# Optimization experiments

Hardware: AMD Instinct MI355X
Metric: run time of the kernel (lower is better)

Reference implementation:

```python
import jax, jax.numpy as jnp
import numpy as np

B, N, H = 2, 4096, 1024
HEADS, DHEAD, M = 16, 64, 256
KERNEL_EPS = 1e-3


def setup_inputs() -> dict:
    key = jax.random.key(0)
    ks = jax.random.split(key, 10)
    w = lambda k, shp: jax.random.normal(k, shp, dtype=jnp.float32) * 0.02
    return {
        "hidden_states": jax.random.normal(ks[0], (B, N, H), dtype=jnp.float32),
        "Wq": w(ks[1], (H, H)), "bq": jnp.zeros((H,), jnp.float32),
        "Wk": w(ks[2], (H, H)), "bk": jnp.zeros((H,), jnp.float32),
        "Wv": w(ks[3], (H, H)), "bv": jnp.zeros((H,), jnp.float32),
        "Wo": w(ks[4], (H, H)), "bo": jnp.zeros((H,), jnp.float32),
        "proj": jax.random.normal(ks[5], (M, DHEAD), dtype=jnp.float32),
    }


def _split_heads(x):
    b, n, _ = x.shape
    return x.reshape(b, n, HEADS, DHEAD).transpose(0, 2, 1, 3)  # [b,h,n,d]


def _softmax_kernel(data, proj, is_query):
    # data: [b,h,n,d]; proj: [m,d]
    data_normalizer = DHEAD ** (-0.25)
    data_dash = jnp.einsum('bhnd,md->bhnm', data_normalizer * data, proj)
    diag_data = -0.5 * jnp.sum(data * data, axis=-1, keepdims=True)  # [b,h,n,1]
    if is_query:
        # argmax over a size-1 last dim -> stabilizer == diag_data itself
        stab = diag_data
    else:
        stab = jnp.max(diag_data)
    kernel_out = jnp.exp(diag_data + (data_dash - stab))  # exp kernel: exp(h + x)
    return (M ** (-0.5)) * (kernel_out + KERNEL_EPS)


def _performer_forward(hidden_states, Wq, bq, Wk, bk, Wv, bv, Wo, bo, proj):
    q = _split_heads(jnp.einsum('bni,oi->bno', hidden_states, Wq) + bq)
    k = _split_heads(jnp.einsum('bni,oi->bno', hidden_states, Wk) + bk)
    v = _split_heads(jnp.einsum('bni,oi->bno', hidden_states, Wv) + bv)

    qf = _softmax_kernel(q, proj, is_query=True)   # [b,h,n,m]
    kf = _softmax_kernel(k, proj, is_query=False)  # [b,h,n,m]

    # linear_attention (non-causal FAVOR+)
    k_cumsum = kf.sum(axis=-2)                                   # [b,h,m]
    d_inv = 1.0 / jnp.einsum('bhnm,bhm->bhn', qf, k_cumsum)      # [b,h,n]
    context = jnp.einsum('bhnm,bhne->bhme', kf, v)               # [b,h,m,d]
    out = jnp.einsum('bhme,bhnm,bhn->bhne', context, qf, d_inv)  # [b,h,n,d]

    out = out.transpose(0, 2, 1, 3).reshape(hidden_states.shape[0], -1, H)
    return jnp.einsum('bni,oi->bno', out, Wo) + bo


def reference(hidden_states, Wq, bq, Wk, bk, Wv, bv, Wo, bo, proj):
    return _performer_forward(hidden_states, Wq, bq, Wk, bk, Wv, bv, Wo, bo, proj)
```

## Files before the change

kernel.cpp:

```cpp
#include <hip/hip_runtime.h>
#include <math.h>

#define B_      2
#define N_      4096
#define H_      1024
#define HEADS_  16
#define DH_     64
#define M_      256
#define NSPLIT  8
#define EPAD    80

constexpr float NORMALIZER = 0.35355339059327373f;
constexpr float RATIO      = 0.0625f;
constexpr float KEPS       = 1e-3f;

typedef __bf16 bf16x8 __attribute__((ext_vector_type(8)));
typedef __bf16 bf16x4 __attribute__((ext_vector_type(4)));
typedef float  f32x4  __attribute__((ext_vector_type(4)));

__global__ __launch_bounds__(256) void split_bf16(
    const float* __restrict__ src, __bf16* __restrict__ hi, __bf16* __restrict__ lo)
{
    int i = blockIdx.x * 256 + threadIdx.x;
    float4 v = ((const float4*)src)[i];
    float vv[4] = {v.x, v.y, v.z, v.w};
    bf16x4 h, l;
#pragma unroll
    for (int j = 0; j < 4; ++j) {
        __bf16 hh = (__bf16)vv[j];
        h[j] = hh;
        l[j] = (__bf16)(vv[j] - (float)hh);
    }
    ((bf16x4*)hi)[i] = h;
    ((bf16x4*)lo)[i] = l;
}

__global__ __launch_bounds__(256) void split_w(
    const float* __restrict__ W0, const float* __restrict__ W1,
    const float* __restrict__ W2, const float* __restrict__ W3,
    __bf16* __restrict__ hi, __bf16* __restrict__ lo)
{
    const float* src = W0;
    if (blockIdx.y == 1) src = W1;
    else if (blockIdx.y == 2) src = W2;
    else if (blockIdx.y == 3) src = W3;
    int i = blockIdx.x * 256 + threadIdx.x;
    size_t o = (size_t)blockIdx.y * 262144 + i;
    float4 v = ((const float4*)src)[i];
    float vv[4] = {v.x, v.y, v.z, v.w};
    bf16x4 h, l;
#pragma unroll
    for (int j = 0; j < 4; ++j) {
        __bf16 hh = (__bf16)vv[j];
        h[j] = hh;
        l[j] = (__bf16)(vv[j] - (float)hh);
    }
    ((bf16x4*)hi)[o] = h;
    ((bf16x4*)lo)[o] = l;
}

template<bool BF16OUT>
__global__ __launch_bounds__(512, 4) void gemm_mfma3(
    const __bf16* __restrict__ Ah, const __bf16* __restrict__ Al,
    const __bf16* __restrict__ Bh0, const __bf16* __restrict__ Bl0,
    const __bf16* __restrict__ Bh1, const __bf16* __restrict__ Bl1,
    const __bf16* __restrict__ Bh2, const __bf16* __restrict__ Bl2,
    const float* __restrict__ bi0, const float* __restrict__ bi1, const float* __restrict__ bi2,
    float* __restrict__ C0,
    __bf16* __restrict__ Ch0, __bf16* __restrict__ Cl0,
    __bf16* __restrict__ Ch1, __bf16* __restrict__ Cl1,
    __bf16* __restrict__ Ch2, __bf16* __restrict__ Cl2)
{
    const __bf16* Bh = Bh0; const __bf16* Bl = Bl0; const float* bias = bi0;
    __bf16* Ch = Ch0; __bf16* Cl = Cl0;
    if (blockIdx.z == 1) { Bh = Bh1; Bl = Bl1; bias = bi1; Ch = Ch1; Cl = Cl1; }
    else if (blockIdx.z == 2) { Bh = Bh2; Bl = Bl2; bias = bi2; Ch = Ch2; Cl = Cl2; }

    __shared__ alignas(16) __bf16 lds[2][4][128 * 32];

    const int t    = threadIdx.x;
    const int lane = t & 63;
    const int lm   = lane & 15;
    const int lq   = lane >> 4;
    const int w    = t >> 6;
    const int wm   = (w >> 2) * 64;
    const int wn   = (w & 3) * 32;

    const int wg = blockIdx.x + 8 * blockIdx.y;
    const int sw = (wg & 7) * 64 + (wg >> 3);
    const int n0 = (sw & 7) * 128;
    const int m0 = (sw >> 3) * 128;
    const int K    = 1024;
    const int NK   = 32;

    const int tw = w >> 1;
    const int hw = w & 1;
    const __bf16* mysrc = (tw == 0) ? Ah : (tw == 1) ? Al : (tw == 2) ? Bh : Bl;
    const int     rbase = ((tw < 2) ? m0 : n0) + hw * 64;
    const int rsub   = lane >> 2;
    const int slot   = lane & 3;
    const int schunk = slot ^ ((lane >> 3) & 3);
    const __bf16* gbase = mysrc + (size_t)(rbase + rsub) * K + schunk * 8;

    f32x4 acc[4][2];
#pragma unroll
    for (int i = 0; i < 4; ++i)
#pragma unroll
        for (int j = 0; j < 2; ++j) acc[i][j] = (f32x4){0.f, 0.f, 0.f, 0.f};

    const int swz = (lq ^ ((lm >> 1) & 3)) * 8;

    auto stage = [&](int buf, int k0) {
#pragma unroll
        for (int c = 0; c < 4; ++c) {
            const __bf16* g = gbase + (size_t)c * 16 * K + k0;
            __builtin_amdgcn_global_load_lds(
                (const __attribute__((address_space(1))) void*)g,
                (__attribute__((address_space(3))) void*)&lds[buf][tw][(hw * 64 + c * 16) * 32],
                16, 0, 0);
        }
    };

    auto compute = [&](int p) {
        const __bf16* tAh = lds[p][0];
        const __bf16* tAl = lds[p][1];
        const __bf16* tBh = lds[p][2];
        const __bf16* tBl = lds[p][3];
        bf16x8 bh[2], bl[2];
#pragma unroll
        for (int j = 0; j < 2; ++j) {
            int off = (wn + j * 16 + lm) * 32 + swz;
            bh[j] = *(const bf16x8*)&tBh[off];
            bl[j] = *(const bf16x8*)&tBl[off];
        }
#pragma unroll
        for (int i = 0; i < 4; ++i) {
            int off = (wm + i * 16 + lm) * 32 + swz;
            bf16x8 ah = *(const bf16x8*)&tAh[off];
            bf16x8 al = *(const bf16x8*)&tAl[off];
#pragma unroll
            for (int j = 0; j < 2; ++j) {
                acc[i][j] = __builtin_amdgcn_mfma_f32_16x16x32_bf16(ah, bh[j], acc[i][j], 0, 0, 0);
                acc[i][j] = __builtin_amdgcn_mfma_f32_16x16x32_bf16(al, bh[j], acc[i][j], 0, 0, 0);
                acc[i][j] = __builtin_amdgcn_mfma_f32_16x16x32_bf16(ah, bl[j], acc[i][j], 0, 0, 0);
            }
        }
    };

    stage(0, 0);
    int p = 0;
#pragma unroll 1
    for (int kk = 0; kk < NK - 1; ++kk) {
        stage(p ^ 1, (kk + 1) * 32);
        asm volatile("s_waitcnt vmcnt(4)" ::: "memory");
        asm volatile("s_barrier" ::: "memory");
        compute(p);
        asm volatile("s_barrier" ::: "memory");
        p ^= 1;
    }
    asm volatile("s_waitcnt vmcnt(0)" ::: "memory");
    asm volatile("s_barrier" ::: "memory");
    compute(p);

    float bsr[2];
#pragma unroll
    for (int j = 0; j < 2; ++j) bsr[j] = bias[n0 + wn + j * 16 + lm];
#pragma unroll
    for (int i = 0; i < 4; ++i)
#pragma unroll
        for (int r = 0; r < 4; ++r) {
            int rowm = m0 + wm + i * 16 + lq * 4 + r;
#pragma unroll
            for (int j = 0; j < 2; ++j) {
                int col = n0 + wn + j * 16 + lm;
                float o = acc[i][j][r] + bsr[j];
                if (BF16OUT) {
                    __bf16 hh = (__bf16)o;
                    Ch[(size_t)rowm * 1024 + col] = hh;
                    Cl[(size_t)rowm * 1024 + col] = (__bf16)(o - (float)hh);
                } else {
                    C0[(size_t)rowm * 1024 + col] = o;
                }
            }
        }
}

__global__ __launch_bounds__(256) void diag_kernel(
    const __bf16* __restrict__ Kh, const __bf16* __restrict__ Kl,
    float* __restrict__ diag, float* __restrict__ partials)
{
    int gt = blockIdx.x * 256 + threadIdx.x;
    int r  = gt >> 2;
    int q  = gt & 3;
    const bf16x8* ph = (const bf16x8*)(Kh + (size_t)r * 64 + q * 16);
    const bf16x8* pl = (const bf16x8*)(Kl + (size_t)r * 64 + q * 16);
    float s = 0.f;
#pragma unroll
    for (int i = 0; i < 2; ++i) {
        bf16x8 vh = ph[i], vl = pl[i];
#pragma unroll
        for (int j = 0; j < 8; ++j) {
            float x = (float)vh[j] + (float)vl[j];
            s += x * x;
        }
    }
    s += __shfl_xor(s, 1);
    s += __shfl_xor(s, 2);
    float d = -0.5f * s;
    if (q == 0) {
        int h = r & 15, bn = r >> 4;
        int n = bn & 4095, b = bn >> 12;
        diag[(((size_t)b * 16 + h) << 12) + n] = d;
    }
    __shared__ float red[256];
    red[threadIdx.x] = d;
    __syncthreads();
    for (int s2 = 128; s2 > 0; s2 >>= 1) {
        if (threadIdx.x < s2) red[threadIdx.x] = fmaxf(red[threadIdx.x], red[threadIdx.x + s2]);
        __syncthreads();
    }
    if (threadIdx.x == 0) partials[blockIdx.x] = red[0];
}

__global__ __launch_bounds__(256) void reduce_stab(
    const float* __restrict__ partials, float* __restrict__ stab, int n)
{
    float m = -3.0e38f;
    for (int i = threadIdx.x; i < n; i += 256) m = fmaxf(m, partials[i]);
    __shared__ float red[256];
    red[threadIdx.x] = m;
    __syncthreads();
    for (int s2 = 128; s2 > 0; s2 >>= 1) {
        if (threadIdx.x < s2) red[threadIdx.x] = fmaxf(red[threadIdx.x], red[threadIdx.x + s2]);
        __syncthreads();
    }
    if (threadIdx.x == 0) stab[0] = red[0];
}

__global__ __launch_bounds__(256) void ctx_mfma(
    const __bf16* __restrict__ Kh, const __bf16* __restrict__ Kl,
    const __bf16* __restrict__ Vh, const __bf16* __restrict__ Vl,
    const __bf16* __restrict__ projH, const __bf16* __restrict__ projL,
    const float* __restrict__ diag, const float* __restrict__ stabp,
    float* __restrict__ ctxp)
{
    __shared__ alignas(16) char ldsbuf[59904];
    __shared__ float dg[64];
    __bf16* kfTh = (__bf16*)ldsbuf;
    __bf16* kfTl = kfTh + 9216;
    __bf16* vTh  = kfTl + 9216;
    __bf16* vTl  = vTh + 5760;
    float*  ctxe = (float*)ldsbuf;

    const int t    = threadIdx.x;
    const int lane = t & 63;
    const int w    = t >> 6;
    const int lm   = lane & 15;
    const int lq   = lane >> 4;
    const int bh   = blockIdx.z;
    const int b    = bh >> 4, h = bh & 15;
    const int mh   = blockIdx.y;
    const int slice = blockIdx.x;
    const int mwave = mh * 128 + w * 32;
    const float stab = stabp[0];
    const size_t rowbase = (size_t)b * N_ * H_ + (size_t)h * DH_;
    const float* diag_bh = diag + (size_t)bh * N_;

    for (int idx = t; idx < 16 * 72; idx += 256) {
        int e = 64 + idx / 72, n = idx % 72;
        vTh[e * 72 + n] = (e == 64 && n < 64) ? (__bf16)1.0f : (__bf16)0.0f;
        vTl[e * 72 + n] = (__bf16)0.0f;
    }

    bf16x8 ph[2][2], pl[2][2];
#pragma unroll
    for (int mf = 0; mf < 2; ++mf)
#pragma unroll
        for (int ks = 0; ks < 2; ++ks) {
            size_t pa = (size_t)(mwave + mf * 16 + lm) * 64 + ks * 32 + lq * 8;
            ph[mf][ks] = *(const bf16x8*)(projH + pa);
            pl[mf][ks] = *(const bf16x8*)(projL + pa);
        }

    f32x4 acc[2][5];
#pragma unroll
    for (int mf = 0; mf < 2; ++mf)
#pragma unroll
        for (int ef = 0; ef < 5; ++ef) acc[mf][ef] = (f32x4){0.f, 0.f, 0.f, 0.f};

    const int nl = t >> 2, dc = (t & 3) * 16;
    bf16x8 v0, v1, u0, u1;
    {
        size_t va = rowbase + (size_t)(slice * (N_ / NSPLIT) + nl) * H_ + dc;
        v0 = *(const bf16x8*)(Vh + va);
        v1 = *(const bf16x8*)(Vh + va + 8);
        u0 = *(const bf16x8*)(Vl + va);
        u1 = *(const bf16x8*)(Vl + va + 8);
    }

    for (int tile = 0; tile < 8; ++tile) {
        const int n0 = slice * (N_ / NSPLIT) + tile * 64;
        __syncthreads();

#pragma unroll
        for (int j = 0; j < 8; ++j) {
            vTh[(dc + j) * 72 + nl]     = v0[j];
            vTh[(dc + 8 + j) * 72 + nl] = v1[j];
            vTl[(dc + j) * 72 + nl]     = u0[j];
            vTl[(dc + 8 + j) * 72 + nl] = u1[j];
        }
        if (t < 64) dg[t] = diag_bh[n0 + t] - stab;

        f32x4 dsh[4][2];
#pragma unroll
        for (int nf = 0; nf < 4; ++nf) {
#pragma unroll
            for (int mf = 0; mf < 2; ++mf) dsh[nf][mf] = (f32x4){0.f, 0.f, 0.f, 0.f};
            bf16x8 ah[2], al[2];
#pragma unroll
            for (int ks = 0; ks < 2; ++ks) {
                size_t ka = rowbase + (size_t)(n0 + nf * 16 + lm) * H_ + ks * 32 + lq * 8;
                ah[ks] = *(const bf16x8*)(Kh + ka);
                al[ks] = *(const bf16x8*)(Kl + ka);
            }
#pragma unroll
            for (int mf = 0; mf < 2; ++mf)
#pragma unroll
                for (int ks = 0; ks < 2; ++ks) {
                    dsh[nf][mf] = __builtin_amdgcn_mfma_f32_16x16x32_bf16(ah[ks], ph[mf][ks], dsh[nf][mf], 0, 0, 0);
                    dsh[nf][mf] = __builtin_amdgcn_mfma_f32_16x16x32_bf16(al[ks], ph[mf][ks], dsh[nf][mf], 0, 0, 0);
                    dsh[nf][mf] = __builtin_amdgcn_mfma_f32_16x16x32_bf16(ah[ks], pl[mf][ks], dsh[nf][mf], 0, 0, 0);
                }
        }

        __syncthreads();

        if (tile < 7) {
            size_t va = rowbase + (size_t)(n0 + 64 + nl) * H_ + dc;
            v0 = *(const bf16x8*)(Vh + va);
            v1 = *(const bf16x8*)(Vh + va + 8);
            u0 = *(const bf16x8*)(Vl + va);
            u1 = *(const bf16x8*)(Vl + va + 8);
        }

#pragma unroll
        for (int nf = 0; nf < 4; ++nf) {
            float4 dgv = *(const float4*)&dg[nf * 16 + lq * 4];
            float dga[4] = {dgv.x, dgv.y, dgv.z, dgv.w};
#pragma unroll
            for (int mf = 0; mf < 2; ++mf) {
                int mrow = w * 32 + mf * 16 + lm;
                bf16x4 vh_, vl_;
#pragma unroll
                for (int r = 0; r < 4; ++r) {
                    float kf = RATIO * (__expf(dga[r] + NORMALIZER * dsh[nf][mf][r]) + KEPS);
                    __bf16 hh = (__bf16)kf;
                    vh_[r] = hh;
                    vl_[r] = (__bf16)(kf - (float)hh);
                }
                int nbase = nf * 16 + lq * 4;
                *(bf16x4*)&kfTh[mrow * 72 + nbase] = vh_;
                *(bf16x4*)&kfTl[mrow * 72 + nbase] = vl_;
            }
        }

#pragma unroll
        for (int ks = 0; ks < 2; ++ks) {
#pragma unroll
            for (int mf = 0; mf < 2; ++mf) {
                bf16x8 af = *(const bf16x8*)&kfTh[(w * 32 + mf * 16 + lm) * 72 + ks * 32 + lq * 8];
                bf16x8 afl = *(const bf16x8*)&kfTl[(w * 32 + mf * 16 + lm) * 72 + ks * 32 + lq * 8];
#pragma unroll
                for (int ef = 0; ef < 5; ++ef) {
                    bf16x8 bfh = *(const bf16x8*)&vTh[(ef * 16 + lm) * 72 + ks * 32 + lq * 8];
                    bf16x8 bfl = *(const bf16x8*)&vTl[(ef * 16 + lm) * 72 + ks * 32 + lq * 8];
                    acc[mf][ef] = __builtin_amdgcn_mfma_f32_16x16x32_bf16(af,  bfh, acc[mf][ef], 0, 0, 0);
                    acc[mf][ef] = __builtin_amdgcn_mfma_f32_16x16x32_bf16(afl, bfh, acc[mf][ef], 0, 0, 0);
                    acc[mf][ef] = __builtin_amdgcn_mfma_f32_16x16x32_bf16(af,  bfl, acc[mf][ef], 0, 0, 0);
                }
            }
        }
    }

    __syncthreads();
#pragma unroll
    for (int mf = 0; mf < 2; ++mf)
#pragma unroll
        for (int ef = 0; ef < 5; ++ef)
#pragma unroll
            for (int r = 0; r < 4; ++r) {
                int ml = w * 32 + mf * 16 + lq * 4 + r;
                int e  = ef * 16 + lm;
                ctxe[ml * 81 + e] = acc[mf][ef][r];
            }
    __syncthreads();
    const size_t SLICE = (size_t)(B_ * HEADS_) * EPAD * M_;
    const size_t obase = (size_t)slice * SLICE + (size_t)bh * EPAD * M_;
    for (int i = t; i < EPAD * 128; i += 256) {
        int e = i >> 7, ml = i & 127;
        ctxp[obase + (size_t)e * M_ + mh * 128 + ml] = ctxe[ml * 81 + e];
    }
}

__global__ __launch_bounds__(256) void ctx_reduce(
    const float* __restrict__ ctxp, __bf16* __restrict__ ctxTh, __bf16* __restrict__ ctxTl)
{
    int idx = blockIdx.x * 256 + threadIdx.x;
    const size_t SLICE = (size_t)(B_ * HEADS_) * EPAD * M_;
    float s = 0.f;
#pragma unroll
    for (int k = 0; k < NSPLIT; ++k) s += ctxp[(size_t)k * SLICE + idx];
    __bf16 hh = (__bf16)s;
    ctxTh[idx] = hh;
    ctxTl[idx] = (__bf16)(s - (float)hh);
}

__global__ __launch_bounds__(256) void out_mfma(
    const __bf16* __restrict__ Qh, const __bf16* __restrict__ Ql,
    const __bf16* __restrict__ projH, const __bf16* __restrict__ projL,
    const __bf16* __restrict__ ctxTh, const __bf16* __restrict__ ctxTl,
    __bf16* __restrict__ attnH, __bf16* __restrict__ attnL)
{
    __shared__ alignas(16) __bf16 qfh[4][32][72];
    __shared__ alignas(16) __bf16 qfl[4][32][72];

    const int t    = threadIdx.x;
    const int lane = t & 63;
    const int w    = t >> 6;
    const int lm   = lane & 15;
    const int lq   = lane >> 4;
    const int bh   = blockIdx.y;
    const int b    = bh >> 4, h = bh & 15;
    const int nw   = blockIdx.x * 128 + w * 32;
    const size_t rowbase = (size_t)b * N_ * H_ + (size_t)h * DH_;

    bf16x8 qh_[2][2], ql_[2][2];
#pragma unroll
    for (int nf = 0; nf < 2; ++nf)
#pragma unroll
        for (int ks = 0; ks < 2; ++ks) {
            size_t qa = rowbase + (size_t)(nw + nf * 16 + lm) * H_ + ks * 32 + lq * 8;
            qh_[nf][ks] = *(const bf16x8*)(Qh + qa);
            ql_[nf][ks] = *(const bf16x8*)(Ql + qa);
        }

    const __bf16* cth = ctxTh + (size_t)bh * EPAD * M_;
    const __bf16* ctl = ctxTl + (size_t)bh * EPAD * M_;

    f32x4 accO[2][5];
#pragma unroll
    for (int nf = 0; nf < 2; ++nf)
#pragma unroll
        for (int ef = 0; ef < 5; ++ef) accO[nf][ef] = (f32x4){0.f, 0.f, 0.f, 0.f};

    for (int mc = 0; mc < 4; ++mc) {
        const int m0 = mc * 64;
        f32x4 dsh[2][4];
#pragma unroll
        for (int nf = 0; nf < 2; ++nf)
#pragma unroll
            for (int mf = 0; mf < 4; ++mf) dsh[nf][mf] = (f32x4){0.f, 0.f, 0.f, 0.f};
#pragma unroll
        for (int mf = 0; mf < 4; ++mf)
#pragma unroll
            for (int ks = 0; ks < 2; ++ks) {
                size_t pa = (size_t)(m0 + mf * 16 + lm) * 64 + ks * 32 + lq * 8;
                bf16x8 ph = *(const bf16x8*)(projH + pa);
                bf16x8 pl = *(const bf16x8*)(projL + pa);
#pragma unroll
                for (int nf = 0; nf < 2; ++nf) {
                    dsh[nf][mf] = __builtin_amdgcn_mfma_f32_16x16x32_bf16(qh_[nf][ks], ph, dsh[nf][mf], 0, 0, 0);
                    dsh[nf][mf] = __builtin_amdgcn_mfma_f32_16x16x32_bf16(ql_[nf][ks], ph, dsh[nf][mf], 0, 0, 0);
                    dsh[nf][mf] = __builtin_amdgcn_mfma_f32_16x16x32_bf16(qh_[nf][ks], pl, dsh[nf][mf], 0, 0, 0);
                }
            }
#pragma unroll
        for (int nf = 0; nf < 2; ++nf)
#pragma unroll
            for (int mf = 0; mf < 4; ++mf)
#pragma unroll
                for (int r = 0; r < 4; ++r) {
                    float qf = RATIO * (__expf(NORMALIZER * dsh[nf][mf][r]) + KEPS);
                    __bf16 hh = (__bf16)qf;
                    int nloc = nf * 16 + lq * 4 + r;
                    qfh[w][nloc][mf * 16 + lm] = hh;
                    qfl[w][nloc][mf * 16 + lm] = (__bf16)(qf - (float)hh);
                }
#pragma unroll
        for (int ks = 0; ks < 2; ++ks) {
            bf16x8 af[2], afl[2];
#pragma unroll
            for (int nf = 0; nf < 2; ++nf) {
                af[nf]  = *(const bf16x8*)&qfh[w][nf * 16 + lm][ks * 32 + lq * 8];
                afl[nf] = *(const bf16x8*)&qfl[w][nf * 16 + lm][ks * 32 + lq * 8];
            }
#pragma unroll
            for (int ef = 0; ef < 5; ++ef) {
                size_t ca = (size_t)(ef * 16 + lm) * M_ + m0 + ks * 32 + lq * 8;
                bf16x8 bfh = *(const bf16x8*)(cth + ca);
                bf16x8 bfl = *(const bf16x8*)(ctl + ca);
#pragma unroll
                for (int nf = 0; nf < 2; ++nf) {
                    accO[nf][ef] = __builtin_amdgcn_mfma_f32_16x16x32_bf16(af[nf],  bfh, accO[nf][ef], 0, 0, 0);
                    accO[nf][ef] = __builtin_amdgcn_mfma_f32_16x16x32_bf16(afl[nf], bfh, accO[nf][ef], 0, 0, 0);
                    accO[nf][ef] = __builtin_amdgcn_mfma_f32_16x16x32_bf16(af[nf],  bfl, accO[nf][ef], 0, 0, 0);
                }
            }
        }
    }

#pragma unroll
    for (int nf = 0; nf < 2; ++nf) {
        float dinv[4];
#pragma unroll
        for (int r = 0; r < 4; ++r) {
            float den = __shfl(accO[nf][4][r], lane & 48);
            dinv[r] = 1.f / den;
        }
#pragma unroll
        for (int ef = 0; ef < 4; ++ef)
#pragma unroll
            for (int r = 0; r < 4; ++r) {
                float o = accO[nf][ef][r] * dinv[r];
                __bf16 hh = (__bf16)o;
                size_t oa = rowbase + (size_t)(nw + nf * 16 + lq * 4 + r) * H_ + ef * 16 + lm;
                attnH[oa] = hh;
                attnL[oa] = (__bf16)(o - (float)hh);
            }
    }
}

extern "C" void kernel_launch(void* const* d_in, const int* in_sizes, int n_in,
                              void* d_out, int out_size, void* d_ws, size_t ws_size,
                              hipStream_t stream) {
    const float* hs   = (const float*)d_in[0];
    const float* Wq   = (const float*)d_in[1];
    const float* bq   = (const float*)d_in[2];
    const float* Wk   = (const float*)d_in[3];
    const float* bk   = (const float*)d_in[4];
    const float* Wv   = (const float*)d_in[5];
    const float* bv   = (const float*)d_in[6];
    const float* Wo   = (const float*)d_in[7];
    const float* bo   = (const float*)d_in[8];
    const float* proj = (const float*)d_in[9];
    float* out = (float*)d_out;

    const size_t QSZ = (size_t)B_ * N_ * H_;
    const size_t WSZ = (size_t)H_ * H_;
    const size_t CTXT = (size_t)B_ * HEADS_ * EPAD * M_;

    __bf16* Qh  = (__bf16*)d_ws;
    __bf16* Ql  = Qh + QSZ;
    __bf16* Kh  = Ql + QSZ;
    __bf16* Kl  = Kh + QSZ;
    __bf16* Vh  = Kl + QSZ;
    __bf16* Vl  = Vh + QSZ;
    __bf16* hsH = Vl + QSZ;
    __bf16* hsL = hsH + QSZ;
    __bf16* WH  = hsL + QSZ;
    __bf16* WL  = WH + 4 * WSZ;
    __bf16* projH = WL + 4 * WSZ;
    __bf16* projL = projH + (size_t)M_ * DH_;
    __bf16* ctxTh = projL + (size_t)M_ * DH_;
    __bf16* ctxTl = ctxTh + CTXT;
    float*  diag  = (float*)(ctxTl + CTXT);
    float*  parts = diag + (size_t)B_ * HEADS_ * N_;
    float*  stab  = parts + 2048;
    float*  ctxp  = stab + 16;

    __bf16 *WqH = WH, *WkH = WH + WSZ, *WvH = WH + 2*WSZ, *WoH = WH + 3*WSZ;
    __bf16 *WqL = WL, *WkL = WL + WSZ, *WvL = WL + 2*WSZ, *WoL = WL + 3*WSZ;

    split_bf16<<<QSZ / 4 / 256, 256, 0, stream>>>(hs, hsH, hsL);
    split_w<<<dim3(WSZ / 4 / 256, 4), 256, 0, stream>>>(Wq, Wk, Wv, Wo, WH, WL);
    split_bf16<<<(M_ * DH_) / 4 / 256, 256, 0, stream>>>(proj, projH, projL);

    gemm_mfma3<true><<<dim3(H_ / 128, (B_ * N_) / 128, 3), 512, 0, stream>>>(
        hsH, hsL, WqH, WqL, WkH, WkL, WvH, WvL, bq, bk, bv,
        nullptr, Qh, Ql, Kh, Kl, Vh, Vl);

    diag_kernel<<<2048, 256, 0, stream>>>(Kh, Kl, diag, parts);
    reduce_stab<<<1, 256, 0, stream>>>(parts, stab, 2048);

    ctx_mfma<<<dim3(NSPLIT, 2, B_ * HEADS_), 256, 0, stream>>>(
        Kh, Kl, Vh, Vl, projH, projL, diag, stab, ctxp);

    ctx_reduce<<<(B_ * HEADS_ * EPAD * M_) / 256, 256, 0, stream>>>(ctxp, ctxTh, ctxTl);

    out_mfma<<<dim3(N_ / 128, B_ * HEADS_), 256, 0, stream>>>(
        Qh, Ql, projH, projL, ctxTh, ctxTl, hsH, hsL);

    gemm_mfma3<false><<<dim3(H_ / 128, (B_ * N_) / 128, 1), 512, 0, stream>>>(
        hsH, hsL, WoH, WoL, WoH, WoL, WoH, WoL, bo, bo, bo,
        out, nullptr, nullptr, nullptr, nullptr, nullptr, nullptr);
}
```

Measured before the change: 451.5 us.

## Prefetch K tiles in ctx kernel and stage ctx in LDS for output kernel

In ctx_mfma, the K hi/lo fragments for the next tile are loaded one iteration ahead, alongside the V prefetch, so global load latency overlaps the MFMA and exp work. In out_mfma, the block grows to 512 threads covering 256 rows. The whole per-head ctx hi/lo matrix is copied into LDS once via global_load_lds with an XOR swizzle, so the MFMA loop reads it from LDS instead of issuing repeated global loads per wave. This raises register pressure in ctx_mfma and LDS use in out_mfma (about 80 KB of ctx plus qf buffers), which may cap occupancy.

```diff
diff --git a/kernel.cpp b/kernel.cpp
--- a/kernel.cpp
+++ b/kernel.cpp
@@ -237,7 +237,7 @@
     if (threadIdx.x == 0) stab[0] = red[0];
 }
 
-__global__ __launch_bounds__(256) void ctx_mfma(
+__global__ __launch_bounds__(256, 2) void ctx_mfma(
     const __bf16* __restrict__ Kh, const __bf16* __restrict__ Kl,
     const __bf16* __restrict__ Vh, const __bf16* __restrict__ Vl,
     const __bf16* __restrict__ projH, const __bf16* __restrict__ projL,
@@ -290,12 +290,22 @@
 
     const int nl = t >> 2, dc = (t & 3) * 16;
     bf16x8 v0, v1, u0, u1;
+    bf16x8 kh_p[4][2], kl_p[4][2];
     {
-        size_t va = rowbase + (size_t)(slice * (N_ / NSPLIT) + nl) * H_ + dc;
+        const int nbase = slice * (N_ / NSPLIT);
+        size_t va = rowbase + (size_t)(nbase + nl) * H_ + dc;
         v0 = *(const bf16x8*)(Vh + va);
         v1 = *(const bf16x8*)(Vh + va + 8);
         u0 = *(const bf16x8*)(Vl + va);
         u1 = *(const bf16x8*)(Vl + va + 8);
+#pragma unroll
+        for (int nf = 0; nf < 4; ++nf)
+#pragma unroll
+            for (int ks = 0; ks < 2; ++ks) {
+                size_t ka = rowbase + (size_t)(nbase + nf * 16 + lm) * H_ + ks * 32 + lq * 8;
+                kh_p[nf][ks] = *(const bf16x8*)(Kh + ka);
+                kl_p[nf][ks] = *(const bf16x8*)(Kl + ka);
+            }
     }
 
     for (int tile = 0; tile < 8; ++tile) {
@@ -316,20 +326,13 @@
         for (int nf = 0; nf < 4; ++nf) {
 #pragma unroll
             for (int mf = 0; mf < 2; ++mf) dsh[nf][mf] = (f32x4){0.f, 0.f, 0.f, 0.f};
-            bf16x8 ah[2], al[2];
-#pragma unroll
-            for (int ks = 0; ks < 2; ++ks) {
-                size_t ka = rowbase + (size_t)(n0 + nf * 16 + lm) * H_ + ks * 32 + lq * 8;
-                ah[ks] = *(const bf16x8*)(Kh + ka);
-                al[ks] = *(const bf16x8*)(Kl + ka);
-            }
 #pragma unroll
             for (int mf = 0; mf < 2; ++mf)
 #pragma unroll
                 for (int ks = 0; ks < 2; ++ks) {
-                    dsh[nf][mf] = __builtin_amdgcn_mfma_f32_16x16x32_bf16(ah[ks], ph[mf][ks], dsh[nf][mf], 0, 0, 0);
-                    dsh[nf][mf] = __builtin_amdgcn_mfma_f32_16x16x32_bf16(al[ks], ph[mf][ks], dsh[nf][mf], 0, 0, 0);
-                    dsh[nf][mf] = __builtin_amdgcn_mfma_f32_16x16x32_bf16(ah[ks], pl[mf][ks], dsh[nf][mf], 0, 0, 0);
+                    dsh[nf][mf] = __builtin_amdgcn_mfma_f32_16x16x32_bf16(kh_p[nf][ks], ph[mf][ks], dsh[nf][mf], 0, 0, 0);
+                    dsh[nf][mf] = __builtin_amdgcn_mfma_f32_16x16x32_bf16(kl_p[nf][ks], ph[mf][ks], dsh[nf][mf], 0, 0, 0);
+                    dsh[nf][mf] = __builtin_amdgcn_mfma_f32_16x16x32_bf16(kh_p[nf][ks], pl[mf][ks], dsh[nf][mf], 0, 0, 0);
                 }
         }
 
@@ -341,6 +344,14 @@
             v1 = *(const bf16x8*)(Vh + va + 8);
             u0 = *(const bf16x8*)(Vl + va);
             u1 = *(const bf16x8*)(Vl + va + 8);
+#pragma unroll
+            for (int nf = 0; nf < 4; ++nf)
+#pragma unroll
+                for (int ks = 0; ks < 2; ++ks) {
+                    size_t ka = rowbase + (size_t)(n0 + 64 + nf * 16 + lm) * H_ + ks * 32 + lq * 8;
+                    kh_p[nf][ks] = *(const bf16x8*)(Kh + ka);
+                    kl_p[nf][ks] = *(const bf16x8*)(Kl + ka);
+                }
         }
 
 #pragma unroll
@@ -415,14 +426,16 @@
     ctxTl[idx] = (__bf16)(s - (float)hh);
 }
 
-__global__ __launch_bounds__(256) void out_mfma(
+__global__ __launch_bounds__(512, 2) void out_mfma(
     const __bf16* __restrict__ Qh, const __bf16* __restrict__ Ql,
     const __bf16* __restrict__ projH, const __bf16* __restrict__ projL,
     const __bf16* __restrict__ ctxTh, const __bf16* __restrict__ ctxTl,
     __bf16* __restrict__ attnH, __bf16* __restrict__ attnL)
 {
-    __shared__ alignas(16) __bf16 qfh[4][32][72];
-    __shared__ alignas(16) __bf16 qfl[4][32][72];
+    __shared__ alignas(16) __bf16 ctxLh[80 * 256];
+    __shared__ alignas(16) __bf16 ctxLl[80 * 256];
+    __shared__ alignas(16) __bf16 qfh[8][32][72];
+    __shared__ alignas(16) __bf16 qfl[8][32][72];
 
     const int t    = threadIdx.x;
     const int lane = t & 63;
@@ -431,8 +444,32 @@
     const int lq   = lane >> 4;
     const int bh   = blockIdx.y;
     const int b    = bh >> 4, h = bh & 15;
-    const int nw   = blockIdx.x * 128 + w * 32;
+    const int nw   = blockIdx.x * 256 + w * 32;
     const size_t rowbase = (size_t)b * N_ * H_ + (size_t)h * DH_;
+
+    const __bf16* cth = ctxTh + (size_t)bh * EPAD * M_;
+    const __bf16* ctl = ctxTl + (size_t)bh * EPAD * M_;
+
+    {
+        const int r_in = lane >> 5;
+        const int cp   = lane & 31;
+#pragma unroll
+        for (int c = 0; c < 5; ++c) {
+            int idx = w * 5 + c;
+            int r   = idx * 2 + r_in;
+            int gc  = cp ^ (r & 7);
+            const __bf16* gh = cth + (size_t)r * 256 + gc * 8;
+            const __bf16* gl = ctl + (size_t)r * 256 + gc * 8;
+            __builtin_amdgcn_global_load_lds(
+                (const __attribute__((address_space(1))) void*)gh,
+                (__attribute__((address_space(3))) void*)&ctxLh[idx * 512],
+                16, 0, 0);
+            __builtin_amdgcn_global_load_lds(
+                (const __attribute__((address_space(1))) void*)gl,
+                (__attribute__((address_space(3))) void*)&ctxLl[idx * 512],
+                16, 0, 0);
+        }
+    }
 
     bf16x8 qh_[2][2], ql_[2][2];
 #pragma unroll
@@ -444,8 +481,7 @@
             ql_[nf][ks] = *(const bf16x8*)(Ql + qa);
         }
 
-    const __bf16* cth = ctxTh + (size_t)bh * EPAD * M_;
-    const __bf16* ctl = ctxTl + (size_t)bh * EPAD * M_;
+    __syncthreads();
 
     f32x4 accO[2][5];
 #pragma unroll
@@ -453,6 +489,7 @@
 #pragma unroll
         for (int ef = 0; ef < 5; ++ef) accO[nf][ef] = (f32x4){0.f, 0.f, 0.f, 0.f};
 
+#pragma unroll
     for (int mc = 0; mc < 4; ++mc) {
         const int m0 = mc * 64;
         f32x4 dsh[2][4];
@@ -496,9 +533,11 @@
             }
 #pragma unroll
             for (int ef = 0; ef < 5; ++ef) {
-                size_t ca = (size_t)(ef * 16 + lm) * M_ + m0 + ks * 32 + lq * 8;
-                bf16x8 bfh = *(const bf16x8*)(cth + ca);
-                bf16x8 bfl = *(const bf16x8*)(ctl + ca);
+                int row = ef * 16 + lm;
+                int sc  = ((m0 >> 3) + ks * 4 + lq) ^ (lm & 7);
+                int off = row * 256 + sc * 8;
+                bf16x8 bfh = *(const bf16x8*)&ctxLh[off];
+                bf16x8 bfl = *(const bf16x8*)&ctxLl[off];
 #pragma unroll
                 for (int nf = 0; nf < 2; ++nf) {
                     accO[nf][ef] = __builtin_amdgcn_mfma_f32_16x16x32_bf16(af[nf],  bfh, accO[nf][ef], 0, 0, 0);
@@ -587,7 +626,7 @@
 
     ctx_reduce<<<(B_ * HEADS_ * EPAD * M_) / 256, 256, 0, stream>>>(ctxp, ctxTh, ctxTl);
 
-    out_mfma<<<dim3(N_ / 128, B_ * HEADS_), 256, 0, stream>>>(
+    out_mfma<<<dim3(N_ / 256, B_ * HEADS_), 512, 0, stream>>>(
         Qh, Ql, projH, projL, ctxTh, ctxTl, hsH, hsL);
 
     gemm_mfma3<false><<<dim3(H_ / 128, (B_ * N_) / 128, 1), 512, 0, stream>>>(
```

After: 417.9 us. 7.4% less time.
